# Kernel tuning notes

Measured on AMD Instinct MI355X. Metric: run time of the kernel, lower is better.

The kernel has to match this reference:

```python
import jax, jax.numpy as jnp
import numpy as np

BN_EPS = 1e-5


def setup_inputs() -> dict:
    key = jax.random.key(0)
    ks = jax.random.split(key, 8)
    B, C, H, W = 8, 256, 64, 64
    Ci = 128
    x = jax.random.normal(ks[0], (B, C, H, W), dtype=jnp.float32)
    # 1x1 conv weights stored as [out, in] (kernel size 1 squeezed)
    sc = 1.0 / np.sqrt(C)
    g_w = jax.random.uniform(ks[1], (Ci, C), jnp.float32, -sc, sc)
    g_b = jax.random.uniform(ks[2], (Ci,), jnp.float32, -sc, sc)
    theta_w = jax.random.uniform(ks[3], (Ci, C), jnp.float32, -sc, sc)
    theta_b = jax.random.uniform(ks[4], (Ci,), jnp.float32, -sc, sc)
    phi_w = jax.random.uniform(ks[5], (Ci, C), jnp.float32, -sc, sc)
    phi_b = jax.random.uniform(ks[6], (Ci,), jnp.float32, -sc, sc)
    # W conv: normal(std=0.01) weight, zero bias (per _init_weights)
    W_w = 0.01 * jax.random.normal(ks[7], (C, Ci), dtype=jnp.float32)
    W_b = jnp.zeros((C,), dtype=jnp.float32)
    bn_gamma = jnp.ones((C,), dtype=jnp.float32)
    bn_beta = jnp.zeros((C,), dtype=jnp.float32)
    return {"x": x, "g_w": g_w, "g_b": g_b, "theta_w": theta_w, "theta_b": theta_b,
            "phi_w": phi_w, "phi_b": phi_b, "W_w": W_w, "W_b": W_b,
            "bn_gamma": bn_gamma, "bn_beta": bn_beta}


def reference(x, g_w, g_b, theta_w, theta_b, phi_w, phi_b, W_w, W_b, bn_gamma, bn_beta):
    B, C, H, W = x.shape
    xf = x.reshape(B, C, H * W)                                   # [B, C, N]
    # 1x1 convs == per-position channel GEMMs
    g_x = jnp.einsum('oc,bcn->bon', g_w, xf) + g_b[:, None]        # [B, Ci, N]
    th = jnp.einsum('oc,bcn->bon', theta_w, xf) + theta_b[:, None]
    ph = jnp.einsum('oc,bcn->bon', phi_w, xf) + phi_b[:, None]
    # theta^T phi : [B, N, N] dense attention scores
    f = jnp.einsum('bcn,bcm->bnm', th, ph)
    attn = jax.nn.softmax(f, axis=-1)
    # attention-weighted sum of g values -> [B, Ci, N]
    y = jnp.einsum('bnm,bcm->bcn', attn, g_x)
    # output 1x1 conv + BatchNorm2d (training-mode batch stats)
    wy = jnp.einsum('oc,bcn->bon', W_w, y) + W_b[:, None]          # [B, C, N]
    mean = jnp.mean(wy, axis=(0, 2), keepdims=True)
    var = jnp.var(wy, axis=(0, 2), keepdims=True)
    wy_bn = (wy - mean) * jax.lax.rsqrt(var + BN_EPS)
    wy_bn = wy_bn * bn_gamma[:, None] + bn_beta[:, None]
    z = wy_bn.reshape(B, C, H, W) + x
    return z
```

## Files before the change

kernel.cpp:

```cpp
#include <hip/hip_runtime.h>
#include <hip/hip_bf16.h>
#include <math.h>

#define B_   8
#define C_   256
#define CI_  128
#define N_   4096

typedef unsigned short ushort_t;
typedef unsigned int uint_t;
typedef __attribute__((ext_vector_type(8))) short short8;
typedef __attribute__((ext_vector_type(16))) float floatx16;

#define OFF_W3B  0ull
#define OFF_B3   196608ull
#define OFF_WCB  198144ull
#define OFF_XT   263680ull
#define OFF_THT  17040896ull
#define OFF_PHT  25429504ull
#define OFF_G16  33818112ull
#define OFF_LP   42206720ull
#define OFF_YPB  42468864ull
#define OFF_WY   263680ull
#define OFF_ST   59246080ull

__device__ __forceinline__ ushort_t f2bf(float x) {
  union { float f; uint_t u; } c; c.f = x;
  return (ushort_t)((c.u + 0x7fffu + ((c.u >> 16) & 1u)) >> 16);
}
__device__ __forceinline__ uint_t pkbf(float a, float b) {
  __hip_bfloat162 h = __float22bfloat162_rn(float2{a, b});
  union { __hip_bfloat162 h; uint_t u; } c; c.h = h; return c.u;
}
__device__ __forceinline__ float bf_lo(uint_t u) {
  union { uint_t u; float f; } c; c.u = u << 16; return c.f;
}
__device__ __forceinline__ float bf_hi(uint_t u) {
  union { uint_t u; float f; } c; c.u = u & 0xffff0000u; return c.f;
}
__device__ __forceinline__ void async_copy16(const void* g, void* l) {
  __builtin_amdgcn_global_load_lds(
      (const __attribute__((address_space(1))) unsigned int*)g,
      (__attribute__((address_space(3))) unsigned int*)l, 16, 0, 0);
}

__global__ __launch_bounds__(256) void pack_w(
    const float* __restrict__ g_w, const float* __restrict__ g_b,
    const float* __restrict__ th_w, const float* __restrict__ th_b,
    const float* __restrict__ ph_w, const float* __restrict__ ph_b,
    const float* __restrict__ W_w,
    ushort_t* __restrict__ W3b, float* __restrict__ b3,
    ushort_t* __restrict__ Wc)
{
  int bid = blockIdx.x;
  if (bid < 384) {
    int i = bid * 256 + threadIdx.x;
    int o = i >> 8;
    float v;
    if (o < 128)      v = g_w[i];
    else if (o < 256) v = th_w[i - 128*256];
    else              v = ph_w[i - 256*256];
    W3b[i] = f2bf(v);
    if ((i & 255) == 0)
      b3[o] = (o < 128) ? g_b[o] : (o < 256) ? th_b[o - 128] : ph_b[o - 256];
  } else {
    int j = (bid - 384) * 256 + threadIdx.x;
    Wc[j] = f2bf(W_w[j]);
  }
}

__global__ __launch_bounds__(256) void xcast(
    const float* __restrict__ x, ushort_t* __restrict__ xt)
{
  const int b = blockIdx.z, c0 = blockIdx.y * 64, n0 = blockIdx.x * 64;
  const int tid = threadIdx.x;
  __shared__ float xs[64][65];
  const int nq = (tid & 15) * 4, cr = tid >> 4;
  #pragma unroll
  for (int i = 0; i < 4; ++i) {
    float4 v = *(const float4*)&x[((size_t)b * C_ + c0 + cr + 16*i) * N_ + n0 + nq];
    xs[cr + 16*i][nq] = v.x; xs[cr + 16*i][nq+1] = v.y;
    xs[cr + 16*i][nq+2] = v.z; xs[cr + 16*i][nq+3] = v.w;
  }
  __syncthreads();
  const int n = tid >> 2, cs = (tid & 3) * 16;
  uint_t u[8];
  #pragma unroll
  for (int j = 0; j < 8; ++j)
    u[j] = pkbf(xs[cs + 2*j][n], xs[cs + 2*j + 1][n]);
  ushort_t* dst = &xt[((size_t)b * N_ + n0 + n) * C_ + c0 + cs];
  *(uint4*)dst       = make_uint4(u[0], u[1], u[2], u[3]);
  *(uint4*)(dst + 8) = make_uint4(u[4], u[5], u[6], u[7]);
}

__global__ __launch_bounds__(256, 2) void proj_all(
    const ushort_t* __restrict__ W3b, const float* __restrict__ b3,
    const ushort_t* __restrict__ xt, ushort_t* __restrict__ tht,
    ushort_t* __restrict__ pht, ushort_t* __restrict__ g16)
{
  const int b = blockIdx.z, nb = blockIdx.x, ot = blockIdx.y;
  const int gm = (ot == 2);
  const int o0 = gm ? 0 : (128 + ot * 128);
  const int tid = threadIdx.x, w = tid >> 6, lane = tid & 63;
  const int l31 = lane & 31, h = lane >> 5, xk = l31 & 7;
  __shared__ ushort_t ws_l[128 * 64];
  __shared__ ushort_t xs_l[128 * 64];
  const ushort_t* xb = xt + (size_t)b * N_ * C_;
  const int n0 = nb * 128;
  floatx16 acc[4];
  #pragma unroll
  for (int ct = 0; ct < 4; ++ct)
    #pragma unroll
    for (int r = 0; r < 16; ++r) acc[ct][r] = 0.f;

  const int gr = lane >> 3, gu = lane & 7;
  for (int k0 = 0; k0 < C_; k0 += 64) {
    __syncthreads();
    #pragma unroll
    for (int i = 0; i < 4; ++i) {
      int r = w*32 + i*8 + gr;
      async_copy16(&W3b[(size_t)(o0 + r) * C_ + k0 + ((gu ^ (r & 7)) * 8)],
                   &ws_l[(w*32 + i*8) * 64]);
      async_copy16(&xb[(size_t)(n0 + r) * C_ + k0 + ((gu ^ (r & 7)) * 8)],
                   &xs_l[(w*32 + i*8) * 64]);
    }
    __syncthreads();
    const ushort_t* bmat = gm ? ws_l : xs_l;
    const ushort_t* amat = gm ? xs_l : ws_l;
    #pragma unroll
    for (int kk = 0; kk < 4; ++kk) {
      int fc = ((2*kk + h) ^ xk) * 8;
      short8 bf = *(const short8*)&bmat[(w*32 + l31) * 64 + fc];
      #pragma unroll
      for (int ct = 0; ct < 4; ++ct) {
        short8 af = *(const short8*)&amat[(ct*32 + l31) * 64 + fc];
        acc[ct] = __builtin_amdgcn_mfma_f32_32x32x16_bf16(af, bf, acc[ct], 0, 0, 0);
      }
    }
  }

  if (gm) {
    float bv = b3[w*32 + l31];
    ushort_t* gp = g16 + ((size_t)b * CI_ + w*32 + l31) * N_;
    #pragma unroll
    for (int ct = 0; ct < 4; ++ct)
      #pragma unroll
      for (int rq = 0; rq < 4; ++rq) {
        uint2 d = make_uint2(pkbf(acc[ct][4*rq+0] + bv, acc[ct][4*rq+1] + bv),
                             pkbf(acc[ct][4*rq+2] + bv, acc[ct][4*rq+3] + bv));
        *(uint2*)&gp[n0 + ct*32 + 8*rq + 4*h] = d;
      }
  } else {
    ushort_t* tp = ((ot == 0) ? tht : pht) + ((size_t)b * N_ + n0 + w*32 + l31) * CI_;
    #pragma unroll
    for (int ct = 0; ct < 4; ++ct)
      #pragma unroll
      for (int rq = 0; rq < 4; ++rq) {
        float4 bv = *(const float4*)&b3[o0 + ct*32 + 8*rq + 4*h];
        uint2 d = make_uint2(pkbf(acc[ct][4*rq+0] + bv.x, acc[ct][4*rq+1] + bv.y),
                             pkbf(acc[ct][4*rq+2] + bv.z, acc[ct][4*rq+3] + bv.w));
        *(uint2*)&tp[ct*32 + 8*rq + 4*h] = d;
      }
  }
}

#define LOG2E_  1.442695041f
#define MBIAS_  (-28.85390082f)

__global__ __launch_bounds__(256, 2) void attn_mfma(
    const ushort_t* __restrict__ tht, const ushort_t* __restrict__ pht,
    const ushort_t* __restrict__ g16, ushort_t* __restrict__ yp,
    float* __restrict__ lp)
{
  const int b  = blockIdx.x & 7;
  const int ms = (blockIdx.x >> 3) & 1;
  const int qb = blockIdx.x >> 4;
  const int tid = threadIdx.x, w = tid >> 6, lane = tid & 63;
  const int l31 = lane & 31, h = lane >> 5, xk = l31 & 7;

  __shared__ ushort_t smem[24576];
  ushort_t* phs = smem;
  ushort_t* gs  = smem + 8192;
  ushort_t* Plw = smem + 16384 + w * 2048;

  const int q0w = qb * 128 + w * 32;
  const int m_base = ms * 2048;

  const ushort_t* thb = tht + (size_t)b * N_ * CI_;
  const ushort_t* phb = pht + (size_t)b * N_ * CI_;
  const ushort_t* gbp = g16 + (size_t)b * CI_ * N_;

  short8 tf[8];
  #pragma unroll
  for (int kk = 0; kk < 8; ++kk)
    tf[kk] = *(const short8*)&thb[(size_t)(q0w + l31) * CI_ + kk*16 + h*8];

  floatx16 acc[4];
  #pragma unroll
  for (int ct = 0; ct < 4; ++ct)
    #pragma unroll
    for (int r = 0; r < 16; ++r) acc[ct][r] = 0.f;
  float lpart = 0.f;

  const int phr = lane >> 4, phu = lane & 15;
  const int gr  = lane >> 3, gu  = lane & 7;

  for (int m0 = m_base; m0 < m_base + 2048; m0 += 64) {
    __syncthreads();
    #pragma unroll
    for (int i = 0; i < 4; ++i) {
      int row = w*16 + i*4 + phr;
      async_copy16(&phb[(size_t)(m0 + row) * CI_ + ((phu ^ (row & 7)) * 8)],
                   &phs[(w*16 + i*4) * 128]);
    }
    #pragma unroll
    for (int i = 0; i < 4; ++i) {
      int c = w*32 + i*8 + gr;
      async_copy16(&gbp[(size_t)c * N_ + m0 + ((gu ^ (c & 7)) * 8)],
                   &gs[(w*32 + i*8) * 64]);
    }
    __syncthreads();

    #pragma unroll
    for (int mt = 0; mt < 2; ++mt) {
      floatx16 s;
      #pragma unroll
      for (int r = 0; r < 16; ++r) s[r] = 0.f;
      #pragma unroll
      for (int kk = 0; kk < 8; ++kk) {
        short8 pf = *(const short8*)&phs[(mt*32 + l31) * 128 + (((2*kk + h) ^ xk) * 8)];
        s = __builtin_amdgcn_mfma_f32_32x32x16_bf16(pf, tf[kk], s, 0, 0, 0);
      }
      float ls = 0.f;
      #pragma unroll
      for (int rq = 0; rq < 4; ++rq) {
        float p0 = exp2f(fmaf(s[4*rq+0], LOG2E_, MBIAS_));
        float p1 = exp2f(fmaf(s[4*rq+1], LOG2E_, MBIAS_));
        float p2 = exp2f(fmaf(s[4*rq+2], LOG2E_, MBIAS_));
        float p3 = exp2f(fmaf(s[4*rq+3], LOG2E_, MBIAS_));
        ls += (p0 + p1) + (p2 + p3);
        uint2 d = make_uint2(pkbf(p0, p1), pkbf(p2, p3));
        *(uint2*)&Plw[l31 * 64 + (((mt*4 + rq) ^ xk) * 8) + h*4] = d;
      }
      lpart += ls;
    }

    #pragma unroll
    for (int kk = 0; kk < 4; ++kk) {
      int pc = ((2*kk + h) ^ xk) * 8;
      short8 pfr = *(const short8*)&Plw[l31 * 64 + pc];
      #pragma unroll
      for (int ct = 0; ct < 4; ++ct) {
        short8 gf = *(const short8*)&gs[(ct*32 + l31) * 64 + pc];
        acc[ct] = __builtin_amdgcn_mfma_f32_32x32x16_bf16(gf, pfr, acc[ct], 0, 0, 0);
      }
    }
  }

  float lq = lpart + __shfl_xor(lpart, 32);
  if (h == 0)
    lp[((size_t)ms * 8 + b) * N_ + q0w + l31] = lq;

  __syncthreads();
  ushort_t* tr = smem + w * 4096;
  #pragma unroll
  for (int ct = 0; ct < 4; ++ct)
    #pragma unroll
    for (int rq = 0; rq < 4; ++rq) {
      uint2 d = make_uint2(pkbf(acc[ct][4*rq+0], acc[ct][4*rq+1]),
                           pkbf(acc[ct][4*rq+2], acc[ct][4*rq+3]));
      *(uint2*)&tr[l31 * 128 + ct*32 + 8*rq + 4*h] = d;
    }
  ushort_t* ypb = yp + (((size_t)ms * 8 + b) * N_ + q0w) * CI_;
  #pragma unroll
  for (int itx = 0; itx < 8; ++itx) {
    int row = itx*4 + (lane >> 4);
    int cu  = (lane & 15) * 8;
    uint4 v = *(const uint4*)&tr[row * 128 + cu];
    *(uint4*)&ypb[(size_t)row * CI_ + cu] = v;
  }
}

__global__ __launch_bounds__(256, 2) void wgemm_fused(
    const ushort_t* __restrict__ Wc, const float* __restrict__ Wb,
    const ushort_t* __restrict__ yp, const float* __restrict__ lp,
    float* __restrict__ WY)
{
  const int b = blockIdx.z, nb = blockIdx.x, ot = blockIdx.y;
  const int o0 = ot * 128;
  const int tid = threadIdx.x, w = tid >> 6, lane = tid & 63;
  const int l31 = lane & 31, h = lane >> 5, xk = l31 & 7;
  __shared__ ushort_t ws_l[128 * 64];
  __shared__ ushort_t xs_l[128 * 64];
  const int n0 = nb * 128;
  const size_t PH = (size_t)B_ * N_ * CI_;
  const ushort_t* yp0 = yp + (size_t)b * N_ * CI_;
  const ushort_t* yp1 = yp0 + PH;
  floatx16 acc[4];
  #pragma unroll
  for (int ct = 0; ct < 4; ++ct)
    #pragma unroll
    for (int r = 0; r < 16; ++r) acc[ct][r] = 0.f;

  const int gr = lane >> 3, gu = lane & 7;
  for (int k0 = 0; k0 < CI_; k0 += 64) {
    __syncthreads();
    #pragma unroll
    for (int i = 0; i < 4; ++i) {
      int r = w*32 + i*8 + gr;
      async_copy16(&Wc[(size_t)(o0 + r) * CI_ + k0 + ((gu ^ (r & 7)) * 8)],
                   &ws_l[(w*32 + i*8) * 64]);
      int n = n0 + r;
      size_t src = (size_t)n * CI_ + k0 + ((gu ^ (r & 7)) * 8);
      uint4 a0 = *(const uint4*)&yp0[src];
      uint4 a1 = *(const uint4*)&yp1[src];
      float inv = 1.0f / (lp[(size_t)b * N_ + n] + lp[(size_t)(8 + b) * N_ + n]);
      uint4 o;
      o.x = pkbf((bf_lo(a0.x) + bf_lo(a1.x)) * inv, (bf_hi(a0.x) + bf_hi(a1.x)) * inv);
      o.y = pkbf((bf_lo(a0.y) + bf_lo(a1.y)) * inv, (bf_hi(a0.y) + bf_hi(a1.y)) * inv);
      o.z = pkbf((bf_lo(a0.z) + bf_lo(a1.z)) * inv, (bf_hi(a0.z) + bf_hi(a1.z)) * inv);
      o.w = pkbf((bf_lo(a0.w) + bf_lo(a1.w)) * inv, (bf_hi(a0.w) + bf_hi(a1.w)) * inv);
      *(uint4*)&xs_l[r * 64 + gu * 8] = o;
    }
    __syncthreads();
    #pragma unroll
    for (int kk = 0; kk < 4; ++kk) {
      int fc = ((2*kk + h) ^ xk) * 8;
      short8 bf = *(const short8*)&xs_l[(w*32 + l31) * 64 + fc];
      #pragma unroll
      for (int ct = 0; ct < 4; ++ct) {
        short8 af = *(const short8*)&ws_l[(ct*32 + l31) * 64 + fc];
        acc[ct] = __builtin_amdgcn_mfma_f32_32x32x16_bf16(af, bf, acc[ct], 0, 0, 0);
      }
    }
  }
  const int n = n0 + w*32 + l31;
  #pragma unroll
  for (int ct = 0; ct < 4; ++ct)
    #pragma unroll
    for (int rq = 0; rq < 4; ++rq) {
      float4 bv = *(const float4*)&Wb[o0 + ct*32 + 8*rq + 4*h];
      #pragma unroll
      for (int j = 0; j < 4; ++j) {
        int o = o0 + ct*32 + 8*rq + 4*h + j;
        WY[((size_t)b * C_ + o) * N_ + n] = acc[ct][4*rq + j] + (&bv.x)[j];
      }
    }
}

__global__ __launch_bounds__(256) void bn_stats(
    const float* __restrict__ WY, float* __restrict__ st)
{
  const int o = blockIdx.x;
  const int tid = threadIdx.x;
  float s = 0.f, s2 = 0.f;
  for (int b = 0; b < B_; ++b) {
    const float* p = WY + ((size_t)b * C_ + o) * N_;
    for (int n = tid * 4; n < N_; n += 256 * 4) {
      float4 v = *(const float4*)&p[n];
      s  += v.x + v.y + v.z + v.w;
      s2 += v.x * v.x + v.y * v.y + v.z * v.z + v.w * v.w;
    }
  }
  __shared__ float rs[256], rs2[256];
  rs[tid] = s; rs2[tid] = s2;
  __syncthreads();
  for (int off = 128; off > 0; off >>= 1) {
    if (tid < off) { rs[tid] += rs[tid + off]; rs2[tid] += rs2[tid + off]; }
    __syncthreads();
  }
  if (tid == 0) {
    const float M = (float)(B_ * N_);
    float mean = rs[0] / M;
    float var  = rs2[0] / M - mean * mean;
    st[o] = mean;
    st[256 + o] = rsqrtf(var + 1e-5f);
  }
}

__global__ __launch_bounds__(256) void bn_apply(
    const float* __restrict__ WY, const float* __restrict__ x,
    const float* __restrict__ st, const float* __restrict__ gamma,
    const float* __restrict__ beta, float* __restrict__ out)
{
  size_t i = ((size_t)blockIdx.x * 256 + threadIdx.x) * 4;
  int o = (int)((i >> 12) & 255);
  float4 w  = *(const float4*)&WY[i];
  float4 xv = *(const float4*)&x[i];
  float gsc = gamma[o] * st[256 + o];
  float bb  = beta[o] - st[o] * gsc;
  float4 v;
  v.x = w.x * gsc + bb + xv.x;
  v.y = w.y * gsc + bb + xv.y;
  v.z = w.z * gsc + bb + xv.z;
  v.w = w.w * gsc + bb + xv.w;
  *(float4*)&out[i] = v;
}

extern "C" void kernel_launch(void* const* d_in, const int* in_sizes, int n_in,
                              void* d_out, int out_size, void* d_ws, size_t ws_size,
                              hipStream_t stream)
{
  const float* x       = (const float*)d_in[0];
  const float* g_w     = (const float*)d_in[1];
  const float* g_b     = (const float*)d_in[2];
  const float* theta_w = (const float*)d_in[3];
  const float* theta_b = (const float*)d_in[4];
  const float* phi_w   = (const float*)d_in[5];
  const float* phi_b   = (const float*)d_in[6];
  const float* W_w     = (const float*)d_in[7];
  const float* W_b     = (const float*)d_in[8];
  const float* gamma   = (const float*)d_in[9];
  const float* beta    = (const float*)d_in[10];
  float* out = (float*)d_out;

  char* ws = (char*)d_ws;
  ushort_t* W3b = (ushort_t*)(ws + OFF_W3B);
  float*    b3  = (float*)(ws + OFF_B3);
  ushort_t* Wc  = (ushort_t*)(ws + OFF_WCB);
  ushort_t* xt  = (ushort_t*)(ws + OFF_XT);
  ushort_t* tht = (ushort_t*)(ws + OFF_THT);
  ushort_t* pht = (ushort_t*)(ws + OFF_PHT);
  ushort_t* g16 = (ushort_t*)(ws + OFF_G16);
  float*    lpp = (float*)(ws + OFF_LP);
  ushort_t* ypb = (ushort_t*)(ws + OFF_YPB);
  float*    WY  = (float*)(ws + OFF_WY);
  float*    ST  = (float*)(ws + OFF_ST);

  pack_w<<<512, 256, 0, stream>>>(g_w, g_b, theta_w, theta_b, phi_w, phi_b,
                                  W_w, W3b, b3, Wc);
  xcast<<<dim3(64, 4, 8), 256, 0, stream>>>(x, xt);
  proj_all<<<dim3(32, 3, 8), 256, 0, stream>>>(W3b, b3, xt, tht, pht, g16);
  attn_mfma<<<512, 256, 0, stream>>>(tht, pht, g16, ypb, lpp);
  wgemm_fused<<<dim3(32, 2, 8), 256, 0, stream>>>(Wc, W_b, ypb, lpp, WY);
  bn_stats<<<256, 256, 0, stream>>>(WY, ST);
  bn_apply<<<8192, 256, 0, stream>>>(WY, x, ST, gamma, beta, out);
}
```

Before: 247.2 us.

## Double-buffer phi/g tiles in attention kernel with async prefetch and MFMA priority

The attention kernel now allocates two LDS buffers for the phi and g tiles and issues the async copy of the next 64-key tile before computing on the current one. This overlaps global loads with the MFMA and exp work, and drops one barrier per iteration. It also raises wave priority around the MFMA blocks via s_setprio. LDS use rises from 48KB to 80KB per block, which may limit occupancy below the two blocks per CU requested in launch bounds.

```diff
diff --git a/kernel.cpp b/kernel.cpp
--- a/kernel.cpp
+++ b/kernel.cpp
@@ -178,10 +178,8 @@
   const int tid = threadIdx.x, w = tid >> 6, lane = tid & 63;
   const int l31 = lane & 31, h = lane >> 5, xk = l31 & 7;
 
-  __shared__ ushort_t smem[24576];
-  ushort_t* phs = smem;
-  ushort_t* gs  = smem + 8192;
-  ushort_t* Plw = smem + 16384 + w * 2048;
+  __shared__ ushort_t smem[40960];
+  ushort_t* Plw = smem + 32768 + w * 2048;
 
   const int q0w = qb * 128 + w * 32;
   const int m_base = ms * 2048;
@@ -205,32 +203,48 @@
   const int phr = lane >> 4, phu = lane & 15;
   const int gr  = lane >> 3, gu  = lane & 7;
 
-  for (int m0 = m_base; m0 < m_base + 2048; m0 += 64) {
-    __syncthreads();
-    #pragma unroll
-    for (int i = 0; i < 4; ++i) {
-      int row = w*16 + i*4 + phr;
-      async_copy16(&phb[(size_t)(m0 + row) * CI_ + ((phu ^ (row & 7)) * 8)],
-                   &phs[(w*16 + i*4) * 128]);
-    }
-    #pragma unroll
-    for (int i = 0; i < 4; ++i) {
-      int c = w*32 + i*8 + gr;
-      async_copy16(&gbp[(size_t)c * N_ + m0 + ((gu ^ (c & 7)) * 8)],
-                   &gs[(w*32 + i*8) * 64]);
-    }
-    __syncthreads();
+  #define STAGE_ATTN(m0v, bufv)                                               \
+    {                                                                         \
+      ushort_t* phs_ = smem + (bufv) * 8192;                                  \
+      ushort_t* gs_  = smem + 16384 + (bufv) * 8192;                          \
+      _Pragma("unroll")                                                       \
+      for (int i = 0; i < 4; ++i) {                                           \
+        int row = w*16 + i*4 + phr;                                           \
+        async_copy16(&phb[(size_t)((m0v) + row) * CI_ + ((phu ^ (row & 7)) * 8)], \
+                     &phs_[(w*16 + i*4) * 128]);                              \
+      }                                                                       \
+      _Pragma("unroll")                                                       \
+      for (int i = 0; i < 4; ++i) {                                           \
+        int c = w*32 + i*8 + gr;                                              \
+        async_copy16(&gbp[(size_t)c * N_ + (m0v) + ((gu ^ (c & 7)) * 8)],     \
+                     &gs_[(w*32 + i*8) * 64]);                                \
+      }                                                                       \
+    }
+
+  STAGE_ATTN(m_base, 0);
+  asm volatile("s_waitcnt vmcnt(0)" ::: "memory");
+  __builtin_amdgcn_s_barrier();
+
+  #pragma unroll 2
+  for (int it = 0; it < 32; ++it) {
+    const int cur = it & 1;
+    const int m0 = m_base + it * 64;
+    if (it < 31) STAGE_ATTN(m0 + 64, cur ^ 1);
+    const ushort_t* phs = smem + cur * 8192;
+    const ushort_t* gs  = smem + 16384 + cur * 8192;
 
     #pragma unroll
     for (int mt = 0; mt < 2; ++mt) {
       floatx16 s;
       #pragma unroll
       for (int r = 0; r < 16; ++r) s[r] = 0.f;
+      __builtin_amdgcn_s_setprio(1);
       #pragma unroll
       for (int kk = 0; kk < 8; ++kk) {
         short8 pf = *(const short8*)&phs[(mt*32 + l31) * 128 + (((2*kk + h) ^ xk) * 8)];
         s = __builtin_amdgcn_mfma_f32_32x32x16_bf16(pf, tf[kk], s, 0, 0, 0);
       }
+      __builtin_amdgcn_s_setprio(0);
       float ls = 0.f;
       #pragma unroll
       for (int rq = 0; rq < 4; ++rq) {
@@ -245,6 +259,7 @@
       lpart += ls;
     }
 
+    __builtin_amdgcn_s_setprio(1);
     #pragma unroll
     for (int kk = 0; kk < 4; ++kk) {
       int pc = ((2*kk + h) ^ xk) * 8;
@@ -255,6 +270,10 @@
         acc[ct] = __builtin_amdgcn_mfma_f32_32x32x16_bf16(gf, pfr, acc[ct], 0, 0, 0);
       }
     }
+    __builtin_amdgcn_s_setprio(0);
+
+    asm volatile("s_waitcnt vmcnt(0)" ::: "memory");
+    __builtin_amdgcn_s_barrier();
   }
 
   float lq = lpart + __shfl_xor(lpart, 32);
```

After: 243.4 us. About the same (-1.5%).
